# Optimization experiments

Measured on AMD Instinct MI355X. Metric: run time of the kernel, lower is better.

Reference implementation:

```python
import jax, jax.numpy as jnp
import numpy as np

B, T, C = 2, 2048, 1024
H, DH = 16, 64  # num_heads, dim_head; inner_dim = H*DH = C


def setup_inputs() -> dict:
    key = jax.random.key(0)
    k_x, k_q, k_k, k_v, k_o, k_r = jax.random.split(key, 6)
    scaled = lambda k, shape, fan: (jax.random.normal(k, shape, jnp.float32) / np.sqrt(fan).astype(np.float32))
    x = jax.random.normal(k_x, (B, T, C), jnp.float32)
    Wq = scaled(k_q, (C, H * DH), C)
    Wk = scaled(k_k, (C, H * DH), C)
    Wv = scaled(k_v, (C, H * DH), C)
    Wo = scaled(k_o, (H * DH, C), H * DH)
    bo = jnp.zeros((C,), jnp.float32)
    # learned relative position bias table, indexed by (i - j) in [-(T-1), T-1]
    rel_table = jax.random.normal(k_r, (H, 2 * T - 1), jnp.float32) * 0.02
    # causal mask, broadcast over batch and heads
    mask = jnp.tril(jnp.ones((T, T), bool))[None, None]  # [1,1,T,T]
    return {"x": x, "Wq": Wq, "Wk": Wk, "Wv": Wv, "Wo": Wo, "bo": bo,
            "rel_table": rel_table, "mask": mask}


def reference(x, Wq, Wk, Wv, Wo, bo, rel_table, mask):
    Bx, Tx, Cx = x.shape
    split = lambda t: t.reshape(Bx, Tx, H, DH).transpose(0, 2, 1, 3)  # [B,H,T,DH]
    q = split(x @ Wq) * (DH ** -0.5)
    k = split(x @ Wk)
    v = split(x @ Wv)
    # relative position bias: bias[h,i,j] = rel_table[h, i-j + T-1]
    rel_idx = jnp.arange(Tx)[:, None] - jnp.arange(Tx)[None, :] + (Tx - 1)  # [T,T]
    bias = rel_table[:, rel_idx]  # [H,T,T]
    score = jnp.einsum('bhid,bhjd->bhij', q, k) + bias[None]
    mask_value = -jnp.finfo(score.dtype).max
    score = jnp.where(mask, score, mask_value)
    attn = jax.nn.softmax(score, axis=-1)
    y = jnp.einsum('bhij,bhjd->bhid', attn, v)
    y = y.transpose(0, 2, 1, 3).reshape(Bx, Tx, H * DH)
    return y @ Wo + bo
```

## Files before the change

kernel.cpp:

```cpp
#include <hip/hip_runtime.h>
#include <hip/hip_bf16.h>
#include <stdint.h>


#define T_SEQ 2048
#define NH    16
#define DHD   64
#define CDIM  1024

typedef unsigned short u16;
typedef unsigned int   u32;
typedef __attribute__((ext_vector_type(8))) __bf16 bf16x8;
typedef __attribute__((ext_vector_type(4))) float f32x4;

#define WAITL0   asm volatile("s_waitcnt lgkmcnt(0)" ::: "memory")

__device__ __forceinline__ float bf2f(u16 b){
  union { u32 u; float f; } v; v.u = ((u32)b) << 16; return v.f;
}
__device__ __forceinline__ u16 f2bf(float f){
  union { __bf16 h; u16 u; } v; v.h = (__bf16)f;
  return v.u;
}

__device__ __forceinline__ uint4 load8(const void* p, long elem, int isbf){
  if (isbf) return *(const uint4*)((const u16*)p + elem);
  const float* fp = (const float*)p + elem;
  float4 a = *(const float4*)fp, b = *(const float4*)(fp + 4);
  uint4 r;
  r.x = (u32)f2bf(a.x) | ((u32)f2bf(a.y) << 16);
  r.y = (u32)f2bf(a.z) | ((u32)f2bf(a.w) << 16);
  r.z = (u32)f2bf(b.x) | ((u32)f2bf(b.y) << 16);
  r.w = (u32)f2bf(b.z) | ((u32)f2bf(b.w) << 16);
  return r;
}
__device__ __forceinline__ float loadf(const void* p, long idx, int isbf){
  return isbf ? bf2f(((const u16*)p)[idx]) : ((const float*)p)[idx];
}

__global__ __launch_bounds__(256) void classify(const u32* __restrict__ x,
                                                int* __restrict__ flag){
  __shared__ int cnt[256];
  int c = 0;
#pragma unroll
  for (int i = 0; i < 16; i++){
    u32 w = x[threadIdx.x * 16 + i];
    int e = (w >> 7) & 0xFF;
    c += (e >= 110 && e <= 140);
  }
  cnt[threadIdx.x] = c;
  __syncthreads();
  for (int s = 128; s > 0; s >>= 1){
    if ((int)threadIdx.x < s) cnt[threadIdx.x] += cnt[threadIdx.x + s];
    __syncthreads();
  }
  if (threadIdx.x == 0) *flag = (cnt[0] > 2048) ? 1 : 0;
}

__global__ __launch_bounds__(256) void transposeW(
    const void* __restrict__ w0, const void* __restrict__ w1,
    const void* __restrict__ w2,
    u16* __restrict__ o0, u16* __restrict__ o1, u16* __restrict__ o2,
    const int* __restrict__ flag)
{
  __shared__ u16 tile[64][72];
  const int isbf = *flag;
  const int z = blockIdx.z;
  const void* in = z==0 ? w0 : z==1 ? w1 : w2;
  u16*      out  = z==0 ? o0 : z==1 ? o1 : o2;
  const int tid = threadIdx.x;
  const int r0 = blockIdx.y * 64, c0 = blockIdx.x * 64;
  const int rr = tid >> 3;
  const int cc = (tid & 7) * 8;
#pragma unroll
  for (int rd = 0; rd < 2; rd++){
    int r = rd*32 + rr;
    *(uint4*)&tile[r][cc] = load8(in, (long)(r0 + r)*CDIM + c0 + cc, isbf);
  }
  __syncthreads();
#pragma unroll
  for (int rd = 0; rd < 2; rd++){
    int oc = rd*32 + rr;
    uint4 wv; u32* wp = (u32*)&wv;
#pragma unroll
    for (int t = 0; t < 4; t++){
      u32 lo = tile[cc + 2*t][oc];
      u32 hi = tile[cc + 2*t + 1][oc];
      wp[t] = lo | (hi << 16);
    }
    *(uint4*)(out + (long)(c0 + oc)*CDIM + r0 + cc) = wv;
  }
}

__device__ __forceinline__ void gemm_body(
    const void* __restrict__ A, const u16* __restrict__ BT,
    const void* __restrict__ bias, void* __restrict__ out,
    float scale, int mode, int m0, int n0, int a_isbf, int io_isbf)
{
  __shared__ u16 ldsA[128*32];
  __shared__ u16 ldsB[128*32];
  const int tid = threadIdx.x;
  const int wid = tid >> 6, lane = tid & 63;
  const int col = lane & 15, quad = lane >> 4;
  const int wm = (wid >> 1) * 64, wn = (wid & 1) * 64;

  const int r0s = tid >> 2, g0 = tid & 3;
  const int r1s = r0s + 64;
  const int sl0 = (g0 ^ (r0s & 3)) * 8;
  const int sl1 = (g0 ^ (r1s & 3)) * 8;

  uint4 rA0, rA1, rB0, rB1;
  auto loadAB = [&](int k0){
    rA0 = load8(A, (long)(m0 + r0s)*CDIM + k0 + g0*8, a_isbf);
    rA1 = load8(A, (long)(m0 + r1s)*CDIM + k0 + g0*8, a_isbf);
    rB0 = *(const uint4*)(BT + (long)(n0 + r0s)*CDIM + k0 + g0*8);
    rB1 = *(const uint4*)(BT + (long)(n0 + r1s)*CDIM + k0 + g0*8);
  };
  auto storeAB = [&](){
    *(uint4*)&ldsA[r0s*32 + sl0] = rA0;
    *(uint4*)&ldsA[r1s*32 + sl1] = rA1;
    *(uint4*)&ldsB[r0s*32 + sl0] = rB0;
    *(uint4*)&ldsB[r1s*32 + sl1] = rB1;
  };

  f32x4 acc[4][4] = {};
  const int NK = CDIM / 32;

  loadAB(0);
  storeAB();
  __syncthreads();

  for (int k = 0; k < NK; k++){
    if (k + 1 < NK) loadAB((k + 1) * 32);

    bf16x8 af[4], bfr[4];
#pragma unroll
    for (int mi = 0; mi < 4; mi++){
      const int r = wm + mi*16 + col;
      af[mi] = *(const bf16x8*)&ldsA[r*32 + ((quad ^ (r & 3)) * 8)];
    }
#pragma unroll
    for (int ni = 0; ni < 4; ni++){
      const int r = wn + ni*16 + col;
      bfr[ni] = *(const bf16x8*)&ldsB[r*32 + ((quad ^ (r & 3)) * 8)];
    }
#pragma unroll
    for (int mi = 0; mi < 4; mi++)
#pragma unroll
      for (int ni = 0; ni < 4; ni++)
        acc[mi][ni] = __builtin_amdgcn_mfma_f32_16x16x32_bf16(af[mi], bfr[ni], acc[mi][ni], 0, 0, 0);

    __syncthreads();
    if (k + 1 < NK){
      storeAB();
      __syncthreads();
    }
  }

  if (mode == 2){
#pragma unroll
    for (int ni = 0; ni < 4; ni++){
      const int n = n0 + wn + ni*16 + col;
      const int h = n >> 6, d = n & 63;
#pragma unroll
      for (int mi = 0; mi < 4; mi++){
        const int m = m0 + wm + mi*16 + quad*4;
        const int b = m >> 11, t = m & (T_SEQ-1);
        uint2 pk;
        pk.x = (u32)f2bf(acc[mi][ni][0]) | ((u32)f2bf(acc[mi][ni][1]) << 16);
        pk.y = (u32)f2bf(acc[mi][ni][2]) | ((u32)f2bf(acc[mi][ni][3]) << 16);
        *(uint2*)((u16*)out + ((long)(b*NH + h)*DHD + d)*T_SEQ + t) = pk;
      }
    }
  } else {
#pragma unroll
    for (int ni = 0; ni < 4; ni++){
      const int n = n0 + wn + ni*16 + col;
      const float bv = bias ? loadf(bias, n, io_isbf) : 0.f;
#pragma unroll
      for (int mi = 0; mi < 4; mi++){
#pragma unroll
        for (int r = 0; r < 4; r++){
          const int m = m0 + wm + mi*16 + quad*4 + r;
          const float v = acc[mi][ni][r] * scale + bv;
          if (mode == 0){
            const long idx = (long)m*CDIM + n;
            if (io_isbf) ((u16*)out)[idx] = f2bf(v);
            else         ((float*)out)[idx] = v;
          } else {
            const int b = m >> 11, t = m & (T_SEQ-1), h = n >> 6, d = n & 63;
            ((u16*)out)[((long)(b*NH + h)*T_SEQ + t)*DHD + d] = f2bf(v);
          }
        }
      }
    }
  }
}

__global__ __launch_bounds__(256) void gemm_qkv(
    const void* __restrict__ x,
    const u16* __restrict__ WqT, const u16* __restrict__ WkT, const u16* __restrict__ WvT,
    u16* __restrict__ Qb, u16* __restrict__ Kb, u16* __restrict__ VTb,
    const int* __restrict__ flag)
{
  const int z = blockIdx.z;
  const u16* BT = z==0 ? WqT : z==1 ? WkT : WvT;
  u16*      dst = z==0 ? Qb  : z==1 ? Kb  : VTb;
  const float scale = (z==0) ? 0.125f * 1.44269504f : 1.0f;
  const int mode = (z==2) ? 2 : 1;
  gemm_body(x, BT, nullptr, dst, scale, mode, blockIdx.x*128, blockIdx.y*128, *flag, 1);
}

__global__ __launch_bounds__(256) void gemm_out(
    const u16* __restrict__ Y, const u16* __restrict__ WoT,
    const void* __restrict__ bo, void* __restrict__ out,
    const int* __restrict__ flag)
{
  gemm_body(Y, WoT, bo, out, 1.0f, 0, blockIdx.x*128, blockIdx.y*128, 1, *flag);
}

__global__ __launch_bounds__(256) void attn64(
    const u16* __restrict__ Q, const u16* __restrict__ K, const u16* __restrict__ VT,
    const void* __restrict__ rel, u16* __restrict__ Y,
    const int* __restrict__ flag)
{
  __shared__ u16 ldsK[64*64];
  __shared__ u16 ldsV[64*64];
  __shared__ u16 ldsP[4][16*88];
  __shared__ float ldsBias[2112];

  const int isbf = *flag;
  const int tid = threadIdx.x, wid = tid >> 6, lane = tid & 63;
  const int col = lane & 15, quad = lane >> 4;

  const int l = (int)blockIdx.x;
  const int xcd = l & 7, s = l >> 3;
  const int bh = xcd * 4 + (s & 3);
  const int g = s >> 2, gq = g >> 3, g0 = g & 7;
  const int ti = (gq == 0) ? 31 - g0
               : (gq == 1) ? g0
               : (gq == 2) ? 23 - g0
                           : 8 + g0;
  const int i0 = ti * 64;

  const int h = bh & (NH - 1);
  const int b = bh >> 4;

  const u16* Qh = Q  + (long)bh * T_SEQ * DHD;
  const u16* Kh = K  + (long)bh * T_SEQ * DHD;
  const u16* Vh = VT + (long)bh * DHD * T_SEQ;
  const long relbase = (long)h * (2*T_SEQ - 1) + (T_SEQ - 1);
  const float MLOG = 16.0f * 1.44269504f;

  const int kr0 = tid >> 3, ks = tid & 7;
  const int kr1 = kr0 + 32;
  const int kd0 = (ks ^ (kr0 & 7)) * 8;
  const int kd1 = (ks ^ (kr1 & 7)) * 8;

  uint4 rk0, rk1, rv0, rv1;
  auto loadKV = [&](int j0){
    rk0 = *(const uint4*)(Kh + (long)(j0 + kr0)*DHD + ks*8);
    rk1 = *(const uint4*)(Kh + (long)(j0 + kr1)*DHD + ks*8);
    rv0 = *(const uint4*)(Vh + (long)kr0*T_SEQ + j0 + ks*8);
    rv1 = *(const uint4*)(Vh + (long)kr1*T_SEQ + j0 + ks*8);
  };
  auto storeKV = [&](){
    *(uint4*)&ldsK[kr0*64 + kd0] = rk0;
    *(uint4*)&ldsK[kr1*64 + kd1] = rk1;
    *(uint4*)&ldsV[kr0*64 + kd0] = rv0;
    *(uint4*)&ldsV[kr1*64 + kd1] = rv1;
  };

  const int nbias = i0 + 127;
  for (int t = tid; t < nbias; t += 256)
    ldsBias[t] = loadf(rel, relbase + t - 63, isbf) * 1.44269504f - MLOG;

  bf16x8 qf0, qf1;
  {
    const u16* qp = Qh + (long)(i0 + wid*16 + col)*DHD + quad*8;
    qf0 = *(const bf16x8*)qp;
    qf1 = *(const bf16x8*)(qp + 32);
  }

  f32x4 O[4] = {};
  float lsum[4] = {0.f, 0.f, 0.f, 0.f};
  const int irow = i0 + wid*16 + quad*4;

  loadKV(0);
  storeKV();
  __syncthreads();

  for (int j0 = 0; j0 <= i0; j0 += 64){
    const bool have_next = (j0 + 64 <= i0);
    if (have_next) loadKV(j0 + 64);

    f32x4 s[4] = {};
#pragma unroll
    for (int kb = 0; kb < 2; kb++){
#pragma unroll
      for (int nb = 0; nb < 4; nb++){
        const int row = nb*16 + col;
        const int sl = ((kb*4 + quad) ^ (row & 7)) * 8;
        bf16x8 kf = *(const bf16x8*)&ldsK[row*64 + sl];
        s[nb] = __builtin_amdgcn_mfma_f32_16x16x32_bf16(kb ? qf1 : qf0, kf, s[nb], 0, 0, 0);
      }
    }

    const bool diag = (j0 == i0);
#pragma unroll
    for (int nb = 0; nb < 4; nb++){
      const int j = j0 + nb*16 + col;
      const float* bp = &ldsBias[irow - j + 63];
#pragma unroll
      for (int r = 0; r < 4; r++){
        float arg = s[nb][r] + bp[r];
        if (diag && (j > irow + r)) arg = -1e9f;
        float p;
        asm volatile("v_exp_f32 %0, %1" : "=v"(p) : "v"(arg));
        s[nb][r] = p;
        lsum[r] += p;
      }
    }

    u16* Pw = ldsP[wid];
#pragma unroll
    for (int nb = 0; nb < 4; nb++)
#pragma unroll
      for (int r = 0; r < 4; r++)
        Pw[(quad*4 + r)*88 + nb*16 + col] = f2bf(s[nb][r]);
    WAITL0;

#pragma unroll
    for (int kb = 0; kb < 2; kb++){
      bf16x8 pf = *(const bf16x8*)&Pw[col*88 + kb*32 + quad*8];
#pragma unroll
      for (int nb = 0; nb < 4; nb++){
        const int row = nb*16 + col;
        const int sl = ((kb*4 + quad) ^ (row & 7)) * 8;
        bf16x8 vf = *(const bf16x8*)&ldsV[row*64 + sl];
        O[nb] = __builtin_amdgcn_mfma_f32_16x16x32_bf16(pf, vf, O[nb], 0, 0, 0);
      }
    }

    __syncthreads();
    if (have_next){
      storeKV();
      __syncthreads();
    }
  }

#pragma unroll
  for (int r = 0; r < 4; r++){
    float v = lsum[r];
    v += __shfl_xor(v, 1, 64);
    v += __shfl_xor(v, 2, 64);
    v += __shfl_xor(v, 4, 64);
    v += __shfl_xor(v, 8, 64);
    lsum[r] = v;
  }

#pragma unroll
  for (int nb = 0; nb < 4; nb++){
#pragma unroll
    for (int r = 0; r < 4; r++){
      const int i = irow + r;
      const int d = nb*16 + col;
      Y[((long)(b*T_SEQ + i))*CDIM + h*DHD + d] = f2bf(O[nb][r] / lsum[r]);
    }
  }
}

extern "C" void kernel_launch(void* const* d_in, const int* in_sizes, int n_in,
                              void* d_out, int out_size, void* d_ws, size_t ws_size,
                              hipStream_t stream)
{
  (void)in_sizes; (void)n_in; (void)out_size; (void)ws_size;
  const void* x   = d_in[0];
  const void* Wq  = d_in[1];
  const void* Wk  = d_in[2];
  const void* Wv  = d_in[3];
  const void* Wo  = d_in[4];
  const void* bo  = d_in[5];
  const void* rel = d_in[6];

  char* ws = (char*)d_ws;
  const size_t MB = 1024*1024;
  int* flag = (int*)ws;
  char* base = ws + 256;
  u16* WqT = (u16*)(base + 0*MB);
  u16* WkT = (u16*)(base + 2*MB);
  u16* WvT = (u16*)(base + 4*MB);
  u16* Kb  = (u16*)(base + 6*MB);
  u16* VTb = (u16*)(base + 14*MB);
  u16* Yb  = (u16*)(base + 0*MB);
  u16* WoT = (u16*)(base + 8*MB);
  u16* Qb  = (u16*)d_out;

  dim3 blk(256);
  classify  <<<1, blk, 0, stream>>>((const u32*)x, flag);
  transposeW<<<dim3(16,16,3), blk, 0, stream>>>(Wq, Wk, Wv, WqT, WkT, WvT, flag);
  gemm_qkv  <<<dim3(32,8,3),  blk, 0, stream>>>(x, WqT, WkT, WvT, Qb, Kb, VTb, flag);
  attn64    <<<dim3(1024),  blk, 0, stream>>>(Qb, Kb, VTb, rel, Yb, flag);
  transposeW<<<dim3(16,16,1), blk, 0, stream>>>(Wo, Wo, Wo, WoT, WoT, WoT, flag);
  gemm_out  <<<dim3(32,8),    blk, 0, stream>>>(Yb, WoT, bo, d_out, flag);
}
```

Before: 240.9 us.

## Double-buffer GEMM LDS with direct global-to-LDS loads and pre-converted x

Converts x to bf16 once in a separate kernel so the QKV GEMM reads only bf16 operands. The GEMM mainloop now uses global_load_lds to write tiles straight into double-buffered LDS, dropping the register staging step and one barrier per k-step. This is meant to cut register pressure and overlap the next tile's fetch with MFMA work, at the cost of an extra launch, extra memory traffic for the bf16 copy of x, and twice the LDS footprint. The bf16 x copy is stored in the output buffer region past Q.

```diff
diff --git a/kernel.cpp b/kernel.cpp
--- a/kernel.cpp
+++ b/kernel.cpp
@@ -21,6 +21,12 @@
 __device__ __forceinline__ u16 f2bf(float f){
   union { __bf16 h; u16 u; } v; v.h = (__bf16)f;
   return v.u;
+}
+
+__device__ __forceinline__ void gload_lds16(const u16* g, u16* l){
+  __builtin_amdgcn_global_load_lds(
+      (const __attribute__((address_space(1))) void*)g,
+      (__attribute__((address_space(3))) void*)l, 16, 0, 0);
 }
 
 __device__ __forceinline__ uint4 load8(const void* p, long elem, int isbf){
@@ -57,6 +63,14 @@
   if (threadIdx.x == 0) *flag = (cnt[0] > 2048) ? 1 : 0;
 }
 
+__global__ __launch_bounds__(256) void cvt_x(const void* __restrict__ x,
+                                             u16* __restrict__ xbf,
+                                             const int* __restrict__ flag){
+  const int isbf = *flag;
+  const long i = ((long)blockIdx.x * 256 + threadIdx.x) * 8;
+  *(uint4*)(xbf + i) = load8(x, i, isbf);
+}
+
 __global__ __launch_bounds__(256) void transposeW(
     const void* __restrict__ w0, const void* __restrict__ w1,
     const void* __restrict__ w2,
@@ -93,56 +107,55 @@
 }
 
 __device__ __forceinline__ void gemm_body(
-    const void* __restrict__ A, const u16* __restrict__ BT,
+    const u16* __restrict__ A, const u16* __restrict__ BT,
     const void* __restrict__ bias, void* __restrict__ out,
-    float scale, int mode, int m0, int n0, int a_isbf, int io_isbf)
-{
-  __shared__ u16 ldsA[128*32];
-  __shared__ u16 ldsB[128*32];
+    float scale, int mode, int m0, int n0, int io_isbf)
+{
+  __shared__ u16 ldsA[2][128*32];
+  __shared__ u16 ldsB[2][128*32];
   const int tid = threadIdx.x;
   const int wid = tid >> 6, lane = tid & 63;
   const int col = lane & 15, quad = lane >> 4;
   const int wm = (wid >> 1) * 64, wn = (wid & 1) * 64;
 
-  const int r0s = tid >> 2, g0 = tid & 3;
-  const int r1s = r0s + 64;
-  const int sl0 = (g0 ^ (r0s & 3)) * 8;
-  const int sl1 = (g0 ^ (r1s & 3)) * 8;
-
-  uint4 rA0, rA1, rB0, rB1;
-  auto loadAB = [&](int k0){
-    rA0 = load8(A, (long)(m0 + r0s)*CDIM + k0 + g0*8, a_isbf);
-    rA1 = load8(A, (long)(m0 + r1s)*CDIM + k0 + g0*8, a_isbf);
-    rB0 = *(const uint4*)(BT + (long)(n0 + r0s)*CDIM + k0 + g0*8);
-    rB1 = *(const uint4*)(BT + (long)(n0 + r1s)*CDIM + k0 + g0*8);
-  };
-  auto storeAB = [&](){
-    *(uint4*)&ldsA[r0s*32 + sl0] = rA0;
-    *(uint4*)&ldsA[r1s*32 + sl1] = rA1;
-    *(uint4*)&ldsB[r0s*32 + sl0] = rB0;
-    *(uint4*)&ldsB[r1s*32 + sl1] = rB1;
+  const int c0 = wid*128 + lane, c1 = c0 + 64;
+  const int r0c = c0 >> 2, g0c = c0 & 3;
+  const int r1c = c1 >> 2, g1c = c1 & 3;
+  const long aoff0 = (long)r0c*CDIM + ((g0c ^ (r0c & 3)) << 3);
+  const long aoff1 = (long)r1c*CDIM + ((g1c ^ (r1c & 3)) << 3);
+  const int lds0 = (wid*128)*8;
+  const int lds1 = (wid*128 + 64)*8;
+
+  const u16* gA = A  + (long)m0*CDIM;
+  const u16* gB = BT + (long)n0*CDIM;
+
+  auto stage = [&](int buf, int k0){
+    gload_lds16(gA + k0 + aoff0, &ldsA[buf][lds0]);
+    gload_lds16(gA + k0 + aoff1, &ldsA[buf][lds1]);
+    gload_lds16(gB + k0 + aoff0, &ldsB[buf][lds0]);
+    gload_lds16(gB + k0 + aoff1, &ldsB[buf][lds1]);
   };
 
   f32x4 acc[4][4] = {};
   const int NK = CDIM / 32;
 
-  loadAB(0);
-  storeAB();
+  stage(0, 0);
   __syncthreads();
 
+  int cur = 0;
   for (int k = 0; k < NK; k++){
-    if (k + 1 < NK) loadAB((k + 1) * 32);
+    if (k + 1 < NK) stage(cur ^ 1, (k + 1) * 32);
 
     bf16x8 af[4], bfr[4];
 #pragma unroll
     for (int mi = 0; mi < 4; mi++){
       const int r = wm + mi*16 + col;
-      af[mi] = *(const bf16x8*)&ldsA[r*32 + ((quad ^ (r & 3)) * 8)];
+      af[mi] = *(const bf16x8*)&ldsA[cur][r*32 + ((quad ^ (r & 3)) * 8)];
     }
 #pragma unroll
     for (int ni = 0; ni < 4; ni++){
       const int r = wn + ni*16 + col;
-      bfr[ni] = *(const bf16x8*)&ldsB[r*32 + ((quad ^ (r & 3)) * 8)];
+      bfr[ni] = *(const bf16x8*)&ldsB[cur][r*32 + ((quad ^ (r & 3)) * 8)];
     }
 #pragma unroll
     for (int mi = 0; mi < 4; mi++)
@@ -151,10 +164,7 @@
         acc[mi][ni] = __builtin_amdgcn_mfma_f32_16x16x32_bf16(af[mi], bfr[ni], acc[mi][ni], 0, 0, 0);
 
     __syncthreads();
-    if (k + 1 < NK){
-      storeAB();
-      __syncthreads();
-    }
+    cur ^= 1;
   }
 
   if (mode == 2){
@@ -198,17 +208,16 @@
 }
 
 __global__ __launch_bounds__(256) void gemm_qkv(
-    const void* __restrict__ x,
+    const u16* __restrict__ xbf,
     const u16* __restrict__ WqT, const u16* __restrict__ WkT, const u16* __restrict__ WvT,
-    u16* __restrict__ Qb, u16* __restrict__ Kb, u16* __restrict__ VTb,
-    const int* __restrict__ flag)
+    u16* __restrict__ Qb, u16* __restrict__ Kb, u16* __restrict__ VTb)
 {
   const int z = blockIdx.z;
   const u16* BT = z==0 ? WqT : z==1 ? WkT : WvT;
   u16*      dst = z==0 ? Qb  : z==1 ? Kb  : VTb;
   const float scale = (z==0) ? 0.125f * 1.44269504f : 1.0f;
   const int mode = (z==2) ? 2 : 1;
-  gemm_body(x, BT, nullptr, dst, scale, mode, blockIdx.x*128, blockIdx.y*128, *flag, 1);
+  gemm_body(xbf, BT, nullptr, dst, scale, mode, blockIdx.x*128, blockIdx.y*128, 1);
 }
 
 __global__ __launch_bounds__(256) void gemm_out(
@@ -216,7 +225,7 @@
     const void* __restrict__ bo, void* __restrict__ out,
     const int* __restrict__ flag)
 {
-  gemm_body(Y, WoT, bo, out, 1.0f, 0, blockIdx.x*128, blockIdx.y*128, 1, *flag);
+  gemm_body(Y, WoT, bo, out, 1.0f, 0, blockIdx.x*128, blockIdx.y*128, *flag);
 }
 
 __global__ __launch_bounds__(256) void attn64(
@@ -395,11 +404,13 @@
   u16* Yb  = (u16*)(base + 0*MB);
   u16* WoT = (u16*)(base + 8*MB);
   u16* Qb  = (u16*)d_out;
+  u16* xbf = Qb + 4u*1024*1024;
 
   dim3 blk(256);
   classify  <<<1, blk, 0, stream>>>((const u32*)x, flag);
+  cvt_x     <<<dim3(2048), blk, 0, stream>>>(x, xbf, flag);
   transposeW<<<dim3(16,16,3), blk, 0, stream>>>(Wq, Wk, Wv, WqT, WkT, WvT, flag);
-  gemm_qkv  <<<dim3(32,8,3),  blk, 0, stream>>>(x, WqT, WkT, WvT, Qb, Kb, VTb, flag);
+  gemm_qkv  <<<dim3(32,8,3),  blk, 0, stream>>>(xbf, WqT, WkT, WvT, Qb, Kb, VTb);
   attn64    <<<dim3(1024),  blk, 0, stream>>>(Qb, Kb, VTb, rel, Yb, flag);
   transposeW<<<dim3(16,16,1), blk, 0, stream>>>(Wo, Wo, Wo, WoT, WoT, WoT, flag);
   gemm_out  <<<dim3(32,8),    blk, 0, stream>>>(Yb, WoT, bo, d_out, flag);
```

New measurement: 223.7 us. 1.08x faster.
